# Kernel optimization log

Measured on AMD Instinct MI355X. Metric: run time of the kernel, lower is better.

## Reference

```python
import jax, jax.numpy as jnp
import numpy as np

# ---- static config (Phi-3-small layer 0, blocksparse branch) ----
HIDDEN = 4096
N_HEADS = 32
N_KV = 8
HEAD_DIM = HIDDEN // N_HEADS        # 128
Q_PER_KV = N_HEADS // N_KV          # 4
SEQ = 2048
ROPE_BASE = 1000000.0
POS_SCALE = 1.0
SM_SCALE = 1.0 / HEAD_DIM           # mup scaling, multiplier=1.0
BLOCK = 64
LOCAL_BLOCKS = 16
VERT_STRIDE = 8


def _blocksparse_mask(seq_len):
    """Dense [S,S] bool mask realizing the causal blocksparse pattern:
    query block i attends key block j iff j<=i and (i-j < LOCAL_BLOCKS or (j+1) % VERT_STRIDE == 0),
    with elementwise causality inside blocks. Built once in numpy (static)."""
    nb = seq_len // BLOCK
    qb = np.arange(nb)[:, None]
    kb = np.arange(nb)[None, :]
    bmask = (kb <= qb) & ((qb - kb < LOCAL_BLOCKS) | ((kb + 1) % VERT_STRIDE == 0))
    emask = np.kron(bmask, np.ones((BLOCK, BLOCK), dtype=bool))
    i = np.arange(seq_len)
    emask &= i[:, None] >= i[None, :]
    return jnp.asarray(emask)


def _rope(x, cos, sin):
    # x: [B, S, H, D]; cos/sin: [S, D]
    x1, x2 = jnp.split(x, 2, axis=-1)
    rot = jnp.concatenate([-x2, x1], axis=-1)
    return x * cos[None, :, None, :] + rot * sin[None, :, None, :]


def setup_inputs() -> dict:
    key = jax.random.key(0)
    k1, k2, k3, k4, k5 = jax.random.split(key, 5)
    qkv_out = (N_HEADS + 2 * N_KV) * HEAD_DIM  # 6144
    return {
        "hidden_states": jax.random.normal(k1, (1, SEQ, HIDDEN), dtype=jnp.float32),
        "w_qkv": jax.random.normal(k2, (qkv_out, HIDDEN), dtype=jnp.float32) * 0.02,
        "b_qkv": jnp.zeros((qkv_out,), dtype=jnp.float32),
        "w_dense": jax.random.normal(k3, (HIDDEN, HIDDEN), dtype=jnp.float32) * 0.02,
        "b_dense": jnp.zeros((HIDDEN,), dtype=jnp.float32),
    }


def reference(hidden_states, w_qkv, b_qkv, w_dense, b_dense):
    B, S, _ = hidden_states.shape
    # grouped QKV projection: [B,S,(H+2*KV)*D]
    qkv = jnp.einsum("bsh,oh->bso", hidden_states, w_qkv) + b_qkv
    # group layout: (group, q0..q3, k, v) per kv head
    qkv = qkv.reshape(B, S, N_KV, Q_PER_KV + 2, HEAD_DIM)
    q = qkv[:, :, :, :Q_PER_KV].reshape(B, S, N_HEADS, HEAD_DIM)
    k = qkv[:, :, :, Q_PER_KV]   # [B,S,KV,D]
    v = qkv[:, :, :, Q_PER_KV + 1]
    # rotary embeddings (HF rotate-half style)
    inv_freq = 1.0 / (ROPE_BASE ** (jnp.arange(0, HEAD_DIM, 2, dtype=jnp.float32) / HEAD_DIM))
    t = jnp.arange(S, dtype=jnp.float32) * POS_SCALE
    freqs = jnp.outer(t, inv_freq)               # [S, D/2]
    emb = jnp.concatenate([freqs, freqs], axis=-1)
    cos, sin = jnp.cos(emb), jnp.sin(emb)
    q = _rope(q, cos, sin)
    k = _rope(k, cos, sin)
    # GQA: replicate kv heads to match q heads
    k = jnp.repeat(k, Q_PER_KV, axis=2)          # [B,S,H,D]
    v = jnp.repeat(v, Q_PER_KV, axis=2)
    mask = _blocksparse_mask(S)                  # [S,S] bool
    scores = jnp.einsum("bqhd,bkhd->bhqk", q, k) * SM_SCALE
    scores = jnp.where(mask[None, None], scores, jnp.finfo(scores.dtype).min)
    probs = jax.nn.softmax(scores, axis=-1)
    ctx = jnp.einsum("bhqk,bkhd->bqhd", probs, v).reshape(B, S, HIDDEN)
    out = jnp.einsum("bsh,oh->bso", ctx, w_dense) + b_dense
    return out
```

## Files before the change

kernel.cpp:

```cpp
#include <hip/hip_runtime.h>
#include <hip/hip_bf16.h>

#define SEQ 2048
#define HIDDEN 4096
#define NH 32
#define NKV 8
#define HD 128
#define QKV_OUT 6144
#define QSCALE (0.0078125f * 1.4426950408889634f)

typedef __attribute__((ext_vector_type(8))) short bf16x8;
typedef __attribute__((ext_vector_type(4))) float f32x4;
typedef __attribute__((ext_vector_type(16))) float f32x16;

__device__ inline unsigned short f32_bf16(float f) {
  union { float f; unsigned int u; } v; v.f = f;
  unsigned int r = v.u + 0x7FFFu + ((v.u >> 16) & 1u);
  return (unsigned short)(r >> 16);
}
__device__ inline float bf16_f32(unsigned short u) {
  union { unsigned int u; float f; } v; v.u = (unsigned int)u << 16;
  return v.f;
}
__device__ inline unsigned int pk(float a, float b) {
  union { __hip_bfloat162 h; unsigned int u; } t;
  t.h = __float22bfloat162_rn(make_float2(a, b));
  return t.u;
}
__device__ inline void pswap(unsigned int &a, unsigned int &b) {
  auto r = __builtin_amdgcn_permlane32_swap((int)a, (int)b, false, false);
  a = (unsigned int)r[0]; b = (unsigned int)r[1];
}
__device__ inline float xmax32(float v) {
  int x = __builtin_bit_cast(int, v);
  auto r = __builtin_amdgcn_permlane32_swap(x, x, false, false);
  return fmaxf(__builtin_bit_cast(float, (int)r[0]), __builtin_bit_cast(float, (int)r[1]));
}
__device__ inline float xadd32(float v) {
  int x = __builtin_bit_cast(int, v);
  auto r = __builtin_amdgcn_permlane32_swap(x, x, false, false);
  return __builtin_bit_cast(float, (int)r[0]) + __builtin_bit_cast(float, (int)r[1]);
}

__global__ __launch_bounds__(256) void conv_bf16(const float* __restrict__ in,
                                                 unsigned short* __restrict__ out,
                                                 int n) {
  int i = (blockIdx.x * 256 + threadIdx.x) * 8;
  if (i + 8 > n) return;
  float4 a = *reinterpret_cast<const float4*>(in + i);
  float4 b = *reinterpret_cast<const float4*>(in + i + 4);
  unsigned short t[8];
  t[0] = f32_bf16(a.x); t[1] = f32_bf16(a.y); t[2] = f32_bf16(a.z); t[3] = f32_bf16(a.w);
  t[4] = f32_bf16(b.x); t[5] = f32_bf16(b.y); t[6] = f32_bf16(b.z); t[7] = f32_bf16(b.w);
  *reinterpret_cast<uint4*>(out + i) = *reinterpret_cast<uint4*>(t);
}

__global__ __launch_bounds__(256) void build_tab(float* __restrict__ ct,
                                                 float* __restrict__ st) {
  int idx = blockIdx.x * 256 + threadIdx.x;
  int s = idx >> 6, d = idx & 63;
  float inv = powf(1.0e6f, -(float)d * (1.0f / 64.0f));
  float f = (float)s * inv;
  ct[idx] = cosf(f);
  st[idx] = sinf(f);
}

template <int BM, int CR, int CC, bool OBF>
__global__ __launch_bounds__(512, 2) void gemm9(const unsigned short* __restrict__ A,
                                                const unsigned short* __restrict__ B,
                                                const float* __restrict__ bias,
                                                void* __restrict__ Cp,
                                                int M, int N, int K) {
  constexpr int BN = 256;
  constexpr int MQ = BM / 64;
  constexpr int La = BM / 128;
  constexpr int Lb = 2;
  constexpr int AH = BM * 64;
  constexpr int BUF = 2 * AH + 32768;
  __shared__ __align__(16) char Lds[BUF * 2];

  const int tid = threadIdx.x;
  const int wave = tid >> 6, lane = tid & 63;
  const int wr = wave >> 2, wc = wave & 3;
  const int lrow = lane & 15, lgrp = lane >> 4;

  const int ntx = N / BN;
  const int wg0 = blockIdx.x;
  const int xcd = wg0 & 7, w = wg0 >> 3;
  const int cpb = ntx / CC;
  const int band = xcd / cpb, colc = xcd % cpb;
  const int bm = (band * CR + w / CC) * BM;
  const int bn = (colc * CC + w % CC) * BN;

  const int srow8 = lane >> 3;
  const int scol = ((lane & 7) ^ srow8) * 8;
  const unsigned short* gsrc[2 * La + 2 * Lb];
  int ldsoff[2 * La + 2 * Lb];
#pragma unroll
  for (int u = 0; u < 2; ++u)
#pragma unroll
    for (int j = 0; j < La; ++j) {
      int row = bm + u * (BM / 2) + (wave * La + j) * 8 + srow8;
      gsrc[u * La + j] = A + (size_t)row * K + scol;
      ldsoff[u * La + j] = u * AH + (wave * La + j) * 1024;
    }
#pragma unroll
  for (int u = 0; u < 2; ++u)
#pragma unroll
    for (int j = 0; j < Lb; ++j) {
      int row = bn + u * 128 + (wave * Lb + j) * 8 + srow8;
      gsrc[2 * La + u * Lb + j] = B + (size_t)row * K + scol;
      ldsoff[2 * La + u * Lb + j] = 2 * AH + u * 16384 + (wave * Lb + j) * 1024;
    }

  auto stage = [&](int bufb, int u, int k0) {
    const int lo = (u < 2) ? u * La : 2 * La + (u - 2) * Lb;
    const int nl = (u < 2) ? La : Lb;
#pragma unroll
    for (int j = 0; j < 4; ++j)
      if (j < nl)
        __builtin_amdgcn_global_load_lds(
            (const __attribute__((address_space(1))) unsigned int*)(gsrc[lo + j] + k0),
            (__attribute__((address_space(3))) unsigned int*)(Lds + bufb + ldsoff[lo + j]),
            16, 0, 0);
  };

  const int rsw = (lrow & 7) << 4;
  auto aoff = [&](int mh, int m, int ks) {
    int r = mh * (BM / 4) + m * 16 + lrow;
    return wr * AH + r * 128 + ((ks * 64 + lgrp * 16) ^ rsw);
  };
  auto boff = [&](int nh, int n, int ks) {
    int r = (wc & 1) * 64 + nh * 32 + n * 16 + lrow;
    return 2 * AH + (wc >> 1) * 16384 + r * 128 + ((ks * 64 + lgrp * 16) ^ rsw);
  };

  f32x4 acc[2 * MQ][4] = {};
  bf16x8 af[MQ][2], bf0[2][2], bf1[2][2];

  const int nt = K / 64;
#pragma unroll
  for (int u = 0; u < 4; ++u) stage(0, u, 0);

  for (int t = 0; t < nt; ++t) {
    const int cur = (t & 1) ? BUF : 0;
    const int nxt = cur ^ BUF;
    const bool pf = (t + 1) < nt;
    const int k1 = (t + 1) * 64;
    const char* base = Lds + cur;

    if (pf) stage(nxt, 0, k1);
    if (pf) { if constexpr (La == 2) asm volatile("s_waitcnt vmcnt(2)" ::: "memory");
              else                   asm volatile("s_waitcnt vmcnt(1)" ::: "memory"); }
    else      asm volatile("s_waitcnt vmcnt(0)" ::: "memory");
    __builtin_amdgcn_sched_barrier(0);
    __builtin_amdgcn_s_barrier();
    __builtin_amdgcn_sched_barrier(0);
#pragma unroll
    for (int m = 0; m < MQ; ++m)
#pragma unroll
      for (int ks = 0; ks < 2; ++ks)
        af[m][ks] = *reinterpret_cast<const bf16x8*>(base + aoff(0, m, ks));
#pragma unroll
    for (int n = 0; n < 2; ++n)
#pragma unroll
      for (int ks = 0; ks < 2; ++ks)
        bf0[n][ks] = *reinterpret_cast<const bf16x8*>(base + boff(0, n, ks));
    __builtin_amdgcn_s_setprio(1);
#pragma unroll
    for (int m = 0; m < MQ; ++m)
#pragma unroll
      for (int n = 0; n < 2; ++n)
#pragma unroll
        for (int ks = 0; ks < 2; ++ks)
          acc[m][n] = __builtin_amdgcn_mfma_f32_16x16x32_bf16(af[m][ks], bf0[n][ks], acc[m][n], 0, 0, 0);
    __builtin_amdgcn_s_setprio(0);

    if (pf) stage(nxt, 1, k1);
#pragma unroll
    for (int n = 0; n < 2; ++n)
#pragma unroll
      for (int ks = 0; ks < 2; ++ks)
        bf1[n][ks] = *reinterpret_cast<const bf16x8*>(base + boff(1, n, ks));
    __builtin_amdgcn_s_setprio(1);
#pragma unroll
    for (int m = 0; m < MQ; ++m)
#pragma unroll
      for (int n = 0; n < 2; ++n)
#pragma unroll
        for (int ks = 0; ks < 2; ++ks)
          acc[m][2 + n] = __builtin_amdgcn_mfma_f32_16x16x32_bf16(af[m][ks], bf1[n][ks], acc[m][2 + n], 0, 0, 0);
    __builtin_amdgcn_s_setprio(0);

    if (pf) stage(nxt, 2, k1);
#pragma unroll
    for (int m = 0; m < MQ; ++m)
#pragma unroll
      for (int ks = 0; ks < 2; ++ks)
        af[m][ks] = *reinterpret_cast<const bf16x8*>(base + aoff(1, m, ks));
    __builtin_amdgcn_s_setprio(1);
#pragma unroll
    for (int m = 0; m < MQ; ++m)
#pragma unroll
      for (int n = 0; n < 2; ++n)
#pragma unroll
        for (int ks = 0; ks < 2; ++ks)
          acc[MQ + m][n] = __builtin_amdgcn_mfma_f32_16x16x32_bf16(af[m][ks], bf0[n][ks], acc[MQ + m][n], 0, 0, 0);
    __builtin_amdgcn_s_setprio(0);

    if (pf) stage(nxt, 3, k1);
    __builtin_amdgcn_s_setprio(1);
#pragma unroll
    for (int m = 0; m < MQ; ++m)
#pragma unroll
      for (int n = 0; n < 2; ++n)
#pragma unroll
        for (int ks = 0; ks < 2; ++ks)
          acc[MQ + m][2 + n] = __builtin_amdgcn_mfma_f32_16x16x32_bf16(af[m][ks], bf1[n][ks], acc[MQ + m][2 + n], 0, 0, 0);
    __builtin_amdgcn_s_setprio(0);
  }

#pragma unroll
  for (int ni = 0; ni < 4; ++ni) {
    int col = bn + wc * 64 + ni * 16 + lrow;
    float bv = bias[col];
#pragma unroll
    for (int mi = 0; mi < 2 * MQ; ++mi)
#pragma unroll
      for (int r = 0; r < 4; ++r) {
        int row = bm + wr * (BM / 2) + mi * 16 + lgrp * 4 + r;
        if constexpr (OBF)
          ((unsigned short*)Cp)[(size_t)row * N + col] = f32_bf16(acc[mi][ni][r] + bv);
        else
          ((float*)Cp)[(size_t)row * N + col] = acc[mi][ni][r] + bv;
      }
  }
}

__global__ __launch_bounds__(256) void rope_split(const unsigned short* __restrict__ qkvb,
                                                  const float* __restrict__ ct,
                                                  const float* __restrict__ st,
                                                  unsigned short* __restrict__ Q,
                                                  unsigned short* __restrict__ Kh,
                                                  unsigned short* __restrict__ Vt) {
  int b = blockIdx.x;
  if (b < 5120) {
    int t = b * 256 + threadIdx.x;
    int d8 = (t & 15) * 8;
    int q = t >> 4;
    int s = q / 40;
    int slotg = q - s * 40;
    int g = slotg / 5, slot = slotg - g * 5;
    const unsigned short* base = qkvb + (size_t)s * QKV_OUT + g * 768 + slot * 128;
    bf16x8 x8 = *reinterpret_cast<const bf16x8*>(base + d8);
    bf16x8 r8 = *reinterpret_cast<const bf16x8*>(base + (d8 ^ 64));
    float4 c0 = *reinterpret_cast<const float4*>(ct + s * 64 + (d8 & 63));
    float4 c1 = *reinterpret_cast<const float4*>(ct + s * 64 + (d8 & 63) + 4);
    float4 s0 = *reinterpret_cast<const float4*>(st + s * 64 + (d8 & 63));
    float4 s1 = *reinterpret_cast<const float4*>(st + s * 64 + (d8 & 63) + 4);
    float cc[8] = {c0.x, c0.y, c0.z, c0.w, c1.x, c1.y, c1.z, c1.w};
    float ss[8] = {s0.x, s0.y, s0.z, s0.w, s1.x, s1.y, s1.z, s1.w};
    float sgn = (d8 < 64) ? -1.0f : 1.0f;
    float sc = (slot < 4) ? QSCALE : 1.0f;
    unsigned short o[8];
#pragma unroll
    for (int i = 0; i < 8; ++i) {
      float x = bf16_f32((unsigned short)x8[i]);
      float r = bf16_f32((unsigned short)r8[i]) * sgn;
      o[i] = f32_bf16((x * cc[i] + r * ss[i]) * sc);
    }
    unsigned short* dst = (slot < 4)
        ? Q + ((size_t)(g * 4 + slot) * SEQ + s) * HD + d8
        : Kh + ((size_t)g * SEQ + s) * HD + d8;
    *reinterpret_cast<uint4*>(dst) = *reinterpret_cast<uint4*>(o);
  } else {
    int t2 = (b - 5120) * 256 + threadIdx.x;
    int d = t2 & 127;
    int rest = t2 >> 7;
    int g = rest & 7;
    int s0 = (rest >> 3) * 8;
    const unsigned short* src = qkvb + (size_t)s0 * QKV_OUT + g * 768 + 640 + d;
    unsigned short o[8];
#pragma unroll
    for (int i = 0; i < 8; ++i) o[i] = src[(size_t)i * QKV_OUT];
    *reinterpret_cast<uint4*>(&Vt[((size_t)g * HD + d) * SEQ + s0]) =
        *reinterpret_cast<uint4*>(o);
  }
}

__device__ inline int nextj(int x, int qb) {
  if (x > qb) return -1;
  if (qb - x < 16) return x;
  int v = (x & ~7) + 7;
  int w = qb - 15;
  return v < w ? v : w;
}

__global__ __launch_bounds__(256, 2) void attn32(const unsigned short* __restrict__ Q,
                                                 const unsigned short* __restrict__ Kh,
                                                 const unsigned short* __restrict__ Vt,
                                                 unsigned short* __restrict__ ctx) {
  const int g = blockIdx.x;
  const int y = (int)gridDim.y - 1 - (int)blockIdx.y;
  const int qb = y >> 1, half = y & 1;
  const int Q0 = y * 32;
  const int tid = threadIdx.x;
  const int wave = tid >> 6;
  const int h = g * 4 + wave;
  const int lane = tid & 63;
  const int l31 = lane & 31, hi = lane >> 5;

  __shared__ __align__(16) char Lds[65536];

  auto stage = [&](int bufb, int j) {
#pragma unroll
    for (int i = 0; i < 4; ++i) {
      int row = i * 16 + (tid >> 4);
      const unsigned short* src =
          Kh + ((size_t)(g * SEQ + j * 64 + row)) * HD + ((tid & 15) ^ (row & 15)) * 8;
      __builtin_amdgcn_global_load_lds(
          (const __attribute__((address_space(1))) unsigned int*)src,
          (__attribute__((address_space(3))) unsigned int*)(Lds + bufb + i * 4096 + (tid >> 6) * 1024),
          16, 0, 0);
    }
#pragma unroll
    for (int i = 0; i < 4; ++i) {
      int row = i * 32 + (tid >> 3);
      const unsigned short* src =
          Vt + ((size_t)(g * HD + row)) * SEQ + j * 64 + ((tid & 7) ^ (row & 7)) * 8;
      __builtin_amdgcn_global_load_lds(
          (const __attribute__((address_space(1))) unsigned int*)src,
          (__attribute__((address_space(3))) unsigned int*)(Lds + bufb + 16384 + i * 4096 + (tid >> 6) * 1024),
          16, 0, 0);
    }
  };

  bf16x8 qf[8];
  const unsigned short* qbase = Q + ((size_t)h * SEQ + Q0 + l31) * HD;
#pragma unroll
  for (int kk = 0; kk < 8; ++kk)
    qf[kk] = *reinterpret_cast<const bf16x8*>(qbase + kk * 16 + hi * 8);

  f32x16 ot[4] = {};
  float mrow = -1e30f, lsum = 0.f;

  const int kswz = l31 & 15;
  const int vswz = l31 & 7;

  int j = nextj(0, qb);
  int cur = 0;
  stage(0, j);
  asm volatile("s_waitcnt vmcnt(0)" ::: "memory");
  __builtin_amdgcn_sched_barrier(0);
  __builtin_amdgcn_s_barrier();
  __builtin_amdgcn_sched_barrier(0);

  while (true) {
    const int jn = (j < qb) ? nextj(j + 1, qb) : -1;
    if (jn >= 0) stage(cur ^ 32768, jn);

    const char* kb = Lds + cur;
    const char* vb = Lds + cur + 16384;
    const bool diag = (j == qb);
    const bool short_blk = diag && (half == 0);

    f32x16 st[2] = {};
    __builtin_amdgcn_s_setprio(1);
#pragma unroll
    for (int kk = 0; kk < 8; ++kk) {
      bf16x8 k0 = *reinterpret_cast<const bf16x8*>(
          kb + (size_t)l31 * 256 + (((2 * kk + hi) ^ kswz) * 16));
      st[0] = __builtin_amdgcn_mfma_f32_32x32x16_bf16(k0, qf[kk], st[0], 0, 0, 0);
      if (!short_blk) {
        bf16x8 k1 = *reinterpret_cast<const bf16x8*>(
            kb + (size_t)(32 + l31) * 256 + (((2 * kk + hi) ^ kswz) * 16));
        st[1] = __builtin_amdgcn_mfma_f32_32x32x16_bf16(k1, qf[kk], st[1], 0, 0, 0);
      }
    }
    __builtin_amdgcn_s_setprio(0);

    if (diag) {
      int qrel = half * 32 + l31;
#pragma unroll
      for (int kt = 0; kt < 2; ++kt)
#pragma unroll
        for (int r = 0; r < 16; ++r) {
          int krel = kt * 32 + (r & 3) + 8 * (r >> 2) + 4 * hi;
          if (krel > qrel) st[kt][r] = -1e30f;
        }
    }

    float t16[16];
#pragma unroll
    for (int r = 0; r < 16; ++r) t16[r] = fmaxf(st[0][r], st[1][r]);
#pragma unroll
    for (int sft = 8; sft >= 1; sft >>= 1)
#pragma unroll
      for (int r = 0; r < sft; ++r) t16[r] = fmaxf(t16[r], t16[r + sft]);
    float vm = xmax32(t16[0]);

    if (!__all(vm - mrow <= 8.0f)) {
      float nm = fmaxf(mrow, vm);
      float corr = __builtin_amdgcn_exp2f(mrow - nm);
      lsum *= corr;
#pragma unroll
      for (int dt = 0; dt < 4; ++dt)
#pragma unroll
        for (int r = 0; r < 16; ++r) ot[dt][r] *= corr;
      mrow = nm;
    }

    float s4[4] = {0.f, 0.f, 0.f, 0.f};
#pragma unroll
    for (int kt = 0; kt < 2; ++kt)
#pragma unroll
      for (int r = 0; r < 16; ++r) {
        float p = __builtin_amdgcn_exp2f(st[kt][r] - mrow);
        st[kt][r] = p;
        s4[r & 3] += p;
      }
    lsum += xadd32((s4[0] + s4[1]) + (s4[2] + s4[3]));

    bf16x8 pb[4];
#pragma unroll
    for (int s = 0; s < 4; ++s) {
      int kt = s >> 1, g0 = (s & 1) * 2, g1 = g0 + 1;
      unsigned int a0 = pk(st[kt][4 * g0 + 0], st[kt][4 * g0 + 1]);
      unsigned int a1 = pk(st[kt][4 * g0 + 2], st[kt][4 * g0 + 3]);
      unsigned int b0 = pk(st[kt][4 * g1 + 0], st[kt][4 * g1 + 1]);
      unsigned int b1 = pk(st[kt][4 * g1 + 2], st[kt][4 * g1 + 3]);
      pswap(a0, b0);
      pswap(a1, b1);
      union { unsigned int u[4]; bf16x8 v; } t;
      t.u[0] = a0; t.u[1] = a1; t.u[2] = b0; t.u[3] = b1;
      pb[s] = t.v;
    }

    const int smax = short_blk ? 2 : 4;
    __builtin_amdgcn_s_setprio(1);
#pragma unroll
    for (int dt = 0; dt < 4; ++dt) {
      const char* vrow = vb + (size_t)(dt * 32 + l31) * 128;
#pragma unroll
      for (int s = 0; s < 4; ++s)
        if (s < smax)
          ot[dt] = __builtin_amdgcn_mfma_f32_32x32x16_bf16(
              *reinterpret_cast<const bf16x8*>(vrow + (((2 * s + hi) ^ vswz) * 16)),
              pb[s], ot[dt], 0, 0, 0);
    }
    __builtin_amdgcn_s_setprio(0);

    if (jn < 0) break;
    asm volatile("s_waitcnt vmcnt(0)" ::: "memory");
    __builtin_amdgcn_sched_barrier(0);
    __builtin_amdgcn_s_barrier();
    __builtin_amdgcn_sched_barrier(0);
    j = jn;
    cur ^= 32768;
  }

  __syncthreads();
  char* W = Lds + wave * 8192;
  float inv = 1.0f / lsum;
  const int swz = (l31 & 7) << 4;
#pragma unroll
  for (int dt = 0; dt < 4; ++dt)
#pragma unroll
    for (int gg = 0; gg < 4; ++gg) {
      unsigned int u0 = pk(ot[dt][4 * gg + 0] * inv, ot[dt][4 * gg + 1] * inv);
      unsigned int u1 = pk(ot[dt][4 * gg + 2] * inv, ot[dt][4 * gg + 3] * inv);
      int off = (dt * 64 + gg * 16 + hi * 8) ^ swz;
      *reinterpret_cast<uint2*>(W + l31 * 256 + off) = make_uint2(u0, u1);
    }
#pragma unroll
  for (int i = 0; i < 8; ++i) {
    int row = lane >> 1;
    int t = (lane & 1) * 8 + i;
    bf16x8 vv = *reinterpret_cast<const bf16x8*>(
        W + row * 256 + ((t * 16) ^ ((row & 7) << 4)));
    *reinterpret_cast<bf16x8*>(&ctx[(size_t)(Q0 + row) * HIDDEN + h * HD + t * 8]) = vv;
  }
}

extern "C" void kernel_launch(void* const* d_in, const int* in_sizes, int n_in,
                              void* d_out, int out_size, void* d_ws, size_t ws_size,
                              hipStream_t stream) {
  const float* hidden  = (const float*)d_in[0];
  const float* w_qkv   = (const float*)d_in[1];
  const float* b_qkv   = (const float*)d_in[2];
  const float* w_dense = (const float*)d_in[3];
  const float* b_dense = (const float*)d_in[4];
  float* out = (float*)d_out;

  char* p = (char*)d_ws;
  unsigned short* hid_bf  = (unsigned short*)p; p += (size_t)SEQ * HIDDEN * 2;
  unsigned short* wqkv_bf = (unsigned short*)p; p += (size_t)QKV_OUT * HIDDEN * 2;
  unsigned short* wd_bf   = (unsigned short*)p; p += (size_t)HIDDEN * HIDDEN * 2;
  unsigned short* qkvb    = (unsigned short*)p; p += (size_t)SEQ * QKV_OUT * 2;
  unsigned short* Qb      = (unsigned short*)p; p += (size_t)NH * SEQ * HD * 2;
  unsigned short* Kb      = (unsigned short*)p; p += (size_t)NKV * SEQ * HD * 2;
  unsigned short* Vt      = (unsigned short*)p; p += (size_t)NKV * HD * SEQ * 2;
  float* ct               = (float*)p;          p += (size_t)SEQ * 64 * 4;
  float* st               = (float*)p;          p += (size_t)SEQ * 64 * 4;
  unsigned short* ctx = hid_bf;

  conv_bf16<<<(SEQ * HIDDEN) / 2048, 256, 0, stream>>>(hidden, hid_bf, SEQ * HIDDEN);
  conv_bf16<<<(QKV_OUT * HIDDEN) / 2048, 256, 0, stream>>>(w_qkv, wqkv_bf, QKV_OUT * HIDDEN);
  conv_bf16<<<(HIDDEN * HIDDEN) / 2048, 256, 0, stream>>>(w_dense, wd_bf, HIDDEN * HIDDEN);
  build_tab<<<(SEQ * 64) / 256, 256, 0, stream>>>(ct, st);

  gemm9<256, 4, 6, true>
      <<<dim3((SEQ / 256) * (QKV_OUT / 256)), 512, 0, stream>>>(
          hid_bf, wqkv_bf, b_qkv, qkvb, SEQ, QKV_OUT, HIDDEN);
  rope_split<<<5120 + 1024, 256, 0, stream>>>(qkvb, ct, st, Qb, Kb, Vt);
  attn32<<<dim3(NKV, SEQ / 32), 256, 0, stream>>>(Qb, Kb, Vt, ctx);
  gemm9<128, 8, 4, false>
      <<<dim3((SEQ / 128) * (HIDDEN / 256)), 512, 0, stream>>>(
          ctx, wd_bf, b_dense, out, SEQ, HIDDEN, HIDDEN);
}
```

Measured before the change: 291.6 us.

## Restructure GEMM pipeline: issue full next-tile prefetch upfront with barrier-interleaved phases

Both GEMMs now issue all global-to-LDS loads for the next K tile at the start of each iteration, rather than spreading them across four phases. The wait on those loads moves to the end of the iteration. The LDS layout is simplified to contiguous A and B regions, and each MFMA phase gets s_barrier plus lgkmcnt waits so waves stay in lockstep, ping-pong style. The aim is to overlap memory traffic with a full tile of MFMA work and cut stalls at the loop-top wait. The added barriers may instead introduce synchronisation overhead.

New measurement: 310.0 us. +6.3%, slower.

```diff
diff --git a/kernel.cpp b/kernel.cpp
--- a/kernel.cpp
+++ b/kernel.cpp
@@ -66,18 +66,17 @@
 }
 
 template <int BM, int CR, int CC, bool OBF>
-__global__ __launch_bounds__(512, 2) void gemm9(const unsigned short* __restrict__ A,
+__global__ __launch_bounds__(512, 2) void gemmF(const unsigned short* __restrict__ A,
                                                 const unsigned short* __restrict__ B,
                                                 const float* __restrict__ bias,
                                                 void* __restrict__ Cp,
                                                 int M, int N, int K) {
   constexpr int BN = 256;
   constexpr int MQ = BM / 64;
-  constexpr int La = BM / 128;
-  constexpr int Lb = 2;
-  constexpr int AH = BM * 64;
-  constexpr int BUF = 2 * AH + 32768;
-  __shared__ __align__(16) char Lds[BUF * 2];
+  constexpr int ABYT = BM * 128;
+  constexpr int SB = ABYT + 32768;
+  constexpr int NA = BM / 64;
+  __shared__ __align__(16) char Lds[SB * 2];
 
   const int tid = threadIdx.x;
   const int wave = tid >> 6, lane = tid & 63;
@@ -92,70 +91,63 @@
   const int bm = (band * CR + w / CC) * BM;
   const int bn = (colc * CC + w % CC) * BN;
 
-  const int srow8 = lane >> 3;
-  const int scol = ((lane & 7) ^ srow8) * 8;
-  const unsigned short* gsrc[2 * La + 2 * Lb];
-  int ldsoff[2 * La + 2 * Lb];
-#pragma unroll
-  for (int u = 0; u < 2; ++u)
-#pragma unroll
-    for (int j = 0; j < La; ++j) {
-      int row = bm + u * (BM / 2) + (wave * La + j) * 8 + srow8;
-      gsrc[u * La + j] = A + (size_t)row * K + scol;
-      ldsoff[u * La + j] = u * AH + (wave * La + j) * 1024;
-    }
-#pragma unroll
-  for (int u = 0; u < 2; ++u)
-#pragma unroll
-    for (int j = 0; j < Lb; ++j) {
-      int row = bn + u * 128 + (wave * Lb + j) * 8 + srow8;
-      gsrc[2 * La + u * Lb + j] = B + (size_t)row * K + scol;
-      ldsoff[2 * La + u * Lb + j] = 2 * AH + u * 16384 + (wave * Lb + j) * 1024;
-    }
-
-  auto stage = [&](int bufb, int u, int k0) {
-    const int lo = (u < 2) ? u * La : 2 * La + (u - 2) * Lb;
-    const int nl = (u < 2) ? La : Lb;
+  const int r8 = lane >> 3;
+  const int scol = ((lane & 7) ^ r8) * 8;
+  const unsigned short* gA[NA]; int lA[NA];
+#pragma unroll
+  for (int j = 0; j < NA; ++j) {
+    int row = bm + wave * (BM / 8) + j * 8 + r8;
+    gA[j] = A + (size_t)row * K + scol;
+    lA[j] = wave * (BM / 8) * 128 + j * 1024;
+  }
+  const unsigned short* gB[4]; int lB[4];
+#pragma unroll
+  for (int j = 0; j < 4; ++j) {
+    int row = bn + wave * 32 + j * 8 + r8;
+    gB[j] = B + (size_t)row * K + scol;
+    lB[j] = ABYT + wave * 32 * 128 + j * 1024;
+  }
+
+  auto stage = [&](int t) {
+    const int bufb = (t & 1) * SB;
+    const int k0 = t * 64;
+#pragma unroll
+    for (int j = 0; j < NA; ++j)
+      __builtin_amdgcn_global_load_lds(
+          (const __attribute__((address_space(1))) unsigned int*)(gA[j] + k0),
+          (__attribute__((address_space(3))) unsigned int*)(Lds + bufb + lA[j]), 16, 0, 0);
 #pragma unroll
     for (int j = 0; j < 4; ++j)
-      if (j < nl)
-        __builtin_amdgcn_global_load_lds(
-            (const __attribute__((address_space(1))) unsigned int*)(gsrc[lo + j] + k0),
-            (__attribute__((address_space(3))) unsigned int*)(Lds + bufb + ldsoff[lo + j]),
-            16, 0, 0);
+      __builtin_amdgcn_global_load_lds(
+          (const __attribute__((address_space(1))) unsigned int*)(gB[j] + k0),
+          (__attribute__((address_space(3))) unsigned int*)(Lds + bufb + lB[j]), 16, 0, 0);
   };
 
   const int rsw = (lrow & 7) << 4;
   auto aoff = [&](int mh, int m, int ks) {
-    int r = mh * (BM / 4) + m * 16 + lrow;
-    return wr * AH + r * 128 + ((ks * 64 + lgrp * 16) ^ rsw);
+    return (wr * (BM / 2) + mh * (BM / 4) + m * 16 + lrow) * 128 +
+           ((ks * 64 + lgrp * 16) ^ rsw);
   };
   auto boff = [&](int nh, int n, int ks) {
-    int r = (wc & 1) * 64 + nh * 32 + n * 16 + lrow;
-    return 2 * AH + (wc >> 1) * 16384 + r * 128 + ((ks * 64 + lgrp * 16) ^ rsw);
+    return ABYT + (wc * 64 + nh * 32 + n * 16 + lrow) * 128 +
+           ((ks * 64 + lgrp * 16) ^ rsw);
   };
 
   f32x4 acc[2 * MQ][4] = {};
   bf16x8 af[MQ][2], bf0[2][2], bf1[2][2];
-
   const int nt = K / 64;
-#pragma unroll
-  for (int u = 0; u < 4; ++u) stage(0, u, 0);
+
+  stage(0);
+  asm volatile("s_waitcnt vmcnt(0)" ::: "memory");
+  __builtin_amdgcn_sched_barrier(0);
+  __builtin_amdgcn_s_barrier();
+  __builtin_amdgcn_sched_barrier(0);
 
   for (int t = 0; t < nt; ++t) {
-    const int cur = (t & 1) ? BUF : 0;
-    const int nxt = cur ^ BUF;
+    const char* base = Lds + (t & 1) * SB;
     const bool pf = (t + 1) < nt;
-    const int k1 = (t + 1) * 64;
-    const char* base = Lds + cur;
-
-    if (pf) stage(nxt, 0, k1);
-    if (pf) { if constexpr (La == 2) asm volatile("s_waitcnt vmcnt(2)" ::: "memory");
-              else                   asm volatile("s_waitcnt vmcnt(1)" ::: "memory"); }
-    else      asm volatile("s_waitcnt vmcnt(0)" ::: "memory");
-    __builtin_amdgcn_sched_barrier(0);
-    __builtin_amdgcn_s_barrier();
-    __builtin_amdgcn_sched_barrier(0);
+
+    if (pf) stage(t + 1);
 #pragma unroll
     for (int m = 0; m < MQ; ++m)
 #pragma unroll
@@ -166,6 +158,9 @@
 #pragma unroll
       for (int ks = 0; ks < 2; ++ks)
         bf0[n][ks] = *reinterpret_cast<const bf16x8*>(base + boff(0, n, ks));
+    __builtin_amdgcn_s_barrier();
+    asm volatile("s_waitcnt lgkmcnt(0)" ::: "memory");
+    __builtin_amdgcn_sched_barrier(0);
     __builtin_amdgcn_s_setprio(1);
 #pragma unroll
     for (int m = 0; m < MQ; ++m)
@@ -175,13 +170,16 @@
         for (int ks = 0; ks < 2; ++ks)
           acc[m][n] = __builtin_amdgcn_mfma_f32_16x16x32_bf16(af[m][ks], bf0[n][ks], acc[m][n], 0, 0, 0);
     __builtin_amdgcn_s_setprio(0);
-
-    if (pf) stage(nxt, 1, k1);
+    __builtin_amdgcn_s_barrier();
+
 #pragma unroll
     for (int n = 0; n < 2; ++n)
 #pragma unroll
       for (int ks = 0; ks < 2; ++ks)
         bf1[n][ks] = *reinterpret_cast<const bf16x8*>(base + boff(1, n, ks));
+    __builtin_amdgcn_s_barrier();
+    asm volatile("s_waitcnt lgkmcnt(0)" ::: "memory");
+    __builtin_amdgcn_sched_barrier(0);
     __builtin_amdgcn_s_setprio(1);
 #pragma unroll
     for (int m = 0; m < MQ; ++m)
@@ -191,13 +189,16 @@
         for (int ks = 0; ks < 2; ++ks)
           acc[m][2 + n] = __builtin_amdgcn_mfma_f32_16x16x32_bf16(af[m][ks], bf1[n][ks], acc[m][2 + n], 0, 0, 0);
     __builtin_amdgcn_s_setprio(0);
-
-    if (pf) stage(nxt, 2, k1);
+    __builtin_amdgcn_s_barrier();
+
 #pragma unroll
     for (int m = 0; m < MQ; ++m)
 #pragma unroll
       for (int ks = 0; ks < 2; ++ks)
         af[m][ks] = *reinterpret_cast<const bf16x8*>(base + aoff(1, m, ks));
+    __builtin_amdgcn_s_barrier();
+    asm volatile("s_waitcnt lgkmcnt(0)" ::: "memory");
+    __builtin_amdgcn_sched_barrier(0);
     __builtin_amdgcn_s_setprio(1);
 #pragma unroll
     for (int m = 0; m < MQ; ++m)
@@ -207,8 +208,8 @@
         for (int ks = 0; ks < 2; ++ks)
           acc[MQ + m][n] = __builtin_amdgcn_mfma_f32_16x16x32_bf16(af[m][ks], bf0[n][ks], acc[MQ + m][n], 0, 0, 0);
     __builtin_amdgcn_s_setprio(0);
-
-    if (pf) stage(nxt, 3, k1);
+    __builtin_amdgcn_s_barrier();
+
     __builtin_amdgcn_s_setprio(1);
 #pragma unroll
     for (int m = 0; m < MQ; ++m)
@@ -218,6 +219,12 @@
         for (int ks = 0; ks < 2; ++ks)
           acc[MQ + m][2 + n] = __builtin_amdgcn_mfma_f32_16x16x32_bf16(af[m][ks], bf1[n][ks], acc[MQ + m][2 + n], 0, 0, 0);
     __builtin_amdgcn_s_setprio(0);
+    if (pf) {
+      asm volatile("s_waitcnt vmcnt(0)" ::: "memory");
+      __builtin_amdgcn_sched_barrier(0);
+      __builtin_amdgcn_s_barrier();
+      __builtin_amdgcn_sched_barrier(0);
+    }
   }
 
 #pragma unroll
@@ -509,12 +516,12 @@
   conv_bf16<<<(HIDDEN * HIDDEN) / 2048, 256, 0, stream>>>(w_dense, wd_bf, HIDDEN * HIDDEN);
   build_tab<<<(SEQ * 64) / 256, 256, 0, stream>>>(ct, st);
 
-  gemm9<256, 4, 6, true>
+  gemmF<256, 4, 6, true>
       <<<dim3((SEQ / 256) * (QKV_OUT / 256)), 512, 0, stream>>>(
           hid_bf, wqkv_bf, b_qkv, qkvb, SEQ, QKV_OUT, HIDDEN);
   rope_split<<<5120 + 1024, 256, 0, stream>>>(qkvb, ct, st, Qb, Kb, Vt);
   attn32<<<dim3(NKV, SEQ / 32), 256, 0, stream>>>(Qb, Kb, Vt, ctx);
-  gemm9<128, 8, 4, false>
+  gemmF<128, 8, 4, false>
       <<<dim3((SEQ / 128) * (HIDDEN / 256)), 512, 0, stream>>>(
           ctx, wd_bf, b_dense, out, SEQ, HIDDEN, HIDDEN);
 }
```

## Fuse prep casts and overlap dense-weight cast with QKV GEMM

Applied to the files above, without the earlier changes.

Merges the hidden and QKV-weight bf16 casts plus the RoPE table build into one prep kernel, which removes several launches. The dense-weight cast now runs in 192 extra workgroups appended to the QKV GEMM grid, so it overlaps with the GEMM instead of running serially. The QKV GEMM tile also changes from BM=256 to BM=128, which doubles the workgroup count. The risk is that the extra cast blocks compete with GEMM blocks for CUs and bandwidth, and the smaller tile lowers data reuse.

Result: slower. 299.4 us (+2.7%).

```diff
diff --git a/kernel.cpp b/kernel.cpp
--- a/kernel.cpp
+++ b/kernel.cpp
@@ -42,42 +42,66 @@
   return __builtin_bit_cast(float, (int)r[0]) + __builtin_bit_cast(float, (int)r[1]);
 }
 
-__global__ __launch_bounds__(256) void conv_bf16(const float* __restrict__ in,
-                                                 unsigned short* __restrict__ out,
-                                                 int n) {
-  int i = (blockIdx.x * 256 + threadIdx.x) * 8;
-  if (i + 8 > n) return;
-  float4 a = *reinterpret_cast<const float4*>(in + i);
-  float4 b = *reinterpret_cast<const float4*>(in + i + 4);
+__device__ inline void cast8(const float* __restrict__ in, unsigned short* __restrict__ out) {
+  float4 a = *reinterpret_cast<const float4*>(in);
+  float4 b = *reinterpret_cast<const float4*>(in + 4);
   unsigned short t[8];
   t[0] = f32_bf16(a.x); t[1] = f32_bf16(a.y); t[2] = f32_bf16(a.z); t[3] = f32_bf16(a.w);
   t[4] = f32_bf16(b.x); t[5] = f32_bf16(b.y); t[6] = f32_bf16(b.z); t[7] = f32_bf16(b.w);
-  *reinterpret_cast<uint4*>(out + i) = *reinterpret_cast<uint4*>(t);
-}
-
-__global__ __launch_bounds__(256) void build_tab(float* __restrict__ ct,
-                                                 float* __restrict__ st) {
-  int idx = blockIdx.x * 256 + threadIdx.x;
-  int s = idx >> 6, d = idx & 63;
-  float inv = powf(1.0e6f, -(float)d * (1.0f / 64.0f));
-  float f = (float)s * inv;
-  ct[idx] = cosf(f);
-  st[idx] = sinf(f);
-}
-
-template <int BM, int CR, int CC, bool OBF>
+  *reinterpret_cast<uint4*>(out) = *reinterpret_cast<uint4*>(t);
+}
+
+#define N1 ((size_t)SEQ * HIDDEN / 8)
+#define N2 ((size_t)QKV_OUT * HIDDEN / 8)
+#define N3 ((size_t)SEQ * 64)
+__global__ __launch_bounds__(256) void prep(const float* __restrict__ hid,
+                                            unsigned short* __restrict__ hid_bf,
+                                            const float* __restrict__ wq,
+                                            unsigned short* __restrict__ wq_bf,
+                                            float* __restrict__ ct,
+                                            float* __restrict__ st) {
+  size_t i = (size_t)blockIdx.x * 256 + threadIdx.x;
+  if (i < N1) {
+    cast8(hid + i * 8, hid_bf + i * 8);
+  } else if (i < N1 + N2) {
+    size_t j = (i - N1) * 8;
+    cast8(wq + j, wq_bf + j);
+  } else {
+    size_t j = i - N1 - N2;
+    int s = (int)(j >> 6), d = (int)(j & 63);
+    float inv = powf(1.0e6f, -(float)d * (1.0f / 64.0f));
+    float f = (float)s * inv;
+    ct[j] = cosf(f);
+    st[j] = sinf(f);
+  }
+}
+
+template <int BM, int CR, int CC, bool OBF, bool FC>
 __global__ __launch_bounds__(512, 2) void gemm9(const unsigned short* __restrict__ A,
                                                 const unsigned short* __restrict__ B,
                                                 const float* __restrict__ bias,
                                                 void* __restrict__ Cp,
-                                                int M, int N, int K) {
+                                                int M, int N, int K,
+                                                const float* __restrict__ cw_in,
+                                                unsigned short* __restrict__ cw_out,
+                                                size_t cw_n, int ngemm) {
   constexpr int BN = 256;
   constexpr int MQ = BM / 64;
   constexpr int La = BM / 128;
   constexpr int Lb = 2;
   constexpr int AH = BM * 64;
-  constexpr int BUF = 2 * AH + 32768;
+  constexpr int BUF = AH * 2 + 32768;
   __shared__ __align__(16) char Lds[BUF * 2];
+
+  if constexpr (FC) {
+    if ((int)blockIdx.x >= ngemm) {
+      size_t base = ((size_t)(blockIdx.x - ngemm) * 512 + threadIdx.x) * 8;
+      size_t stride = (size_t)(gridDim.x - ngemm) * 512 * 8;
+      for (size_t i = base; i < cw_n; i += stride)
+        cast8(cw_in + i, cw_out + i);
+      return;
+    }
+  }
 
   const int tid = threadIdx.x;
   const int wave = tid >> 6, lane = tid & 63;
@@ -504,17 +528,18 @@
   float* st               = (float*)p;          p += (size_t)SEQ * 64 * 4;
   unsigned short* ctx = hid_bf;
 
-  conv_bf16<<<(SEQ * HIDDEN) / 2048, 256, 0, stream>>>(hidden, hid_bf, SEQ * HIDDEN);
-  conv_bf16<<<(QKV_OUT * HIDDEN) / 2048, 256, 0, stream>>>(w_qkv, wqkv_bf, QKV_OUT * HIDDEN);
-  conv_bf16<<<(HIDDEN * HIDDEN) / 2048, 256, 0, stream>>>(w_dense, wd_bf, HIDDEN * HIDDEN);
-  build_tab<<<(SEQ * 64) / 256, 256, 0, stream>>>(ct, st);
-
-  gemm9<256, 4, 6, true>
-      <<<dim3((SEQ / 256) * (QKV_OUT / 256)), 512, 0, stream>>>(
-          hid_bf, wqkv_bf, b_qkv, qkvb, SEQ, QKV_OUT, HIDDEN);
+  const int prep_blocks = (int)((N1 + N2 + N3 + 255) / 256);
+  prep<<<prep_blocks, 256, 0, stream>>>(hidden, hid_bf, w_qkv, wqkv_bf, ct, st);
+
+  const int ngemm_qkv = (SEQ / 128) * (QKV_OUT / 256);
+  gemm9<128, 8, 6, true, true>
+      <<<dim3(ngemm_qkv + 192), 512, 0, stream>>>(
+          hid_bf, wqkv_bf, b_qkv, qkvb, SEQ, QKV_OUT, HIDDEN,
+          w_dense, wd_bf, (size_t)HIDDEN * HIDDEN, ngemm_qkv);
   rope_split<<<5120 + 1024, 256, 0, stream>>>(qkvb, ct, st, Qb, Kb, Vt);
   attn32<<<dim3(NKV, SEQ / 32), 256, 0, stream>>>(Qb, Kb, Vt, ctx);
-  gemm9<128, 8, 4, false>
+  gemm9<128, 8, 4, false, false>
       <<<dim3((SEQ / 128) * (HIDDEN / 256)), 512, 0, stream>>>(
-          ctx, wd_bf, b_dense, out, SEQ, HIDDEN, HIDDEN);
-}
+          ctx, wd_bf, b_dense, out, SEQ, HIDDEN, HIDDEN,
+          nullptr, nullptr, 0, 0);
+}
```
